# Optimization experiments

Hardware: AMD Instinct MI355X
Metric: run time of the kernel (lower is better)

The kernel has to match this reference:

```python
import jax, jax.numpy as jnp
import numpy as np

B, C, HH, WW = 256, 1024, 7, 7
S = HH * WW            # 49 tokens
D = 1024               # hidden_size
L = 2                  # encoder_layers (nhead arg, swapped in source)
H = 2                  # attention heads (num_layers arg, swapped in source)
HD = D // H            # 512 head dim
FF = 1024              # encoder_ffn_dim
OUT = 1024             # head output
EPS = 1e-5


def setup_inputs() -> dict:
    key = jax.random.key(0)
    ks = jax.random.split(key, 10)
    n = lambda k, shape: jax.random.normal(k, shape, jnp.float32) * 0.02
    return dict(
        x=jax.random.normal(ks[0], (B, C, HH, WW), jnp.float32),
        pos_emb=n(ks[1], (S, D)),
        ln1_s=jnp.ones((L, D), jnp.float32), ln1_b=jnp.zeros((L, D), jnp.float32),
        wq=n(ks[2], (L, D, D)), wk=n(ks[3], (L, D, D)),
        wv=n(ks[4], (L, D, D)), wo=n(ks[5], (L, D, D)),
        ln2_s=jnp.ones((L, D), jnp.float32), ln2_b=jnp.zeros((L, D), jnp.float32),
        w1=n(ks[6], (L, D, FF)), b1=jnp.zeros((L, FF), jnp.float32),
        w2=n(ks[7], (L, FF, D)), b2=jnp.zeros((L, D), jnp.float32),
        lnf_s=jnp.ones((D,), jnp.float32), lnf_b=jnp.zeros((D,), jnp.float32),
        head_w=n(ks[8], (S * D, OUT)), head_b=jnp.zeros((OUT,), jnp.float32),
    )


def _ln(x, s, b):
    m = jnp.mean(x, axis=-1, keepdims=True)
    v = jnp.var(x, axis=-1, keepdims=True)
    return (x - m) * jax.lax.rsqrt(v + EPS) * s + b


def reference(x, pos_emb, ln1_s, ln1_b, wq, wk, wv, wo, ln2_s, ln2_b,
              w1, b1, w2, b2, lnf_s, lnf_b, head_w, head_b):
    b = x.shape[0]
    # flatten HxW then permute -> [B, S, D] token sequence
    h = x.reshape(b, C, S).transpose(0, 2, 1)
    # BigBirdPegasus encoder: learned pos emb added to inputs_embeds (no scaling path)
    h = h + pos_emb[None, :, :]
    scale = 1.0 / jnp.sqrt(jnp.float32(HD))
    for i in range(L):
        # --- self-attention block (pre-LN); seq_len=49 triggers original_full attention ---
        r = h
        hn = _ln(h, ln1_s[i], ln1_b[i])
        q = (hn @ wq[i]).reshape(b, S, H, HD)
        k = (hn @ wk[i]).reshape(b, S, H, HD)
        v = (hn @ wv[i]).reshape(b, S, H, HD)
        scores = jnp.einsum('bqhd,bkhd->bhqk', q, k) * scale
        attn = jax.nn.softmax(scores, axis=-1)
        ctx = jnp.einsum('bhqk,bkhd->bqhd', attn, v).reshape(b, S, D)
        h = r + ctx @ wo[i]
        # --- feed-forward block (pre-LN, gelu_new) ---
        r = h
        hn = _ln(h, ln2_s[i], ln2_b[i])
        hn = jax.nn.gelu(hn @ w1[i] + b1[i], approximate=True)
        h = r + hn @ w2[i] + b2[i]
    # BigBirdPegasus applies layernorm_embedding AFTER the layer stack
    h = _ln(h, lnf_s, lnf_b)
    # flatten + linear + relu head
    out = jax.nn.relu(h.reshape(b, S * D) @ head_w + head_b)
    return out
```

## Files before the change

kernel.cpp:

```cpp
#include <hip/hip_runtime.h>
#include <hip/hip_bf16.h>
#include <stdint.h>

#define Bq 256
#define Sq 49
#define Dq 1024
#define Hq 2
#define HDq 512
#define Mq (Bq*Sq)
#define KHEADq (Sq*Dq)
#define STq 3072

typedef unsigned short u16;
typedef short bf16x8 __attribute__((ext_vector_type(8)));
typedef float f32x4 __attribute__((ext_vector_type(4)));

__device__ inline u16 f2bf(float f){
  union { float f; uint32_t u; } c; c.f = f;
  uint32_t r = c.u + 0x7FFFu + ((c.u >> 16) & 1u);
  return (u16)(r >> 16);
}
__device__ inline float bf2f(u16 h){
  union { uint32_t u; float f; } c; c.u = ((uint32_t)h) << 16;
  return c.f;
}

#define GLOAD_LDS16(gp, lp) \
  __builtin_amdgcn_global_load_lds((__attribute__((address_space(1))) void*)(gp), \
                                   (__attribute__((address_space(3))) void*)(lp), 16, 0, 0)
#define MFMA16(a,b,c) __builtin_amdgcn_mfma_f32_16x16x32_bf16(a,b,c,0,0,0)

__global__ __launch_bounds__(256) void prep_kernel(const float* __restrict__ x,
    const float* __restrict__ pos, u16* __restrict__ h){
  __shared__ float t[49*129];
  int b = blockIdx.x, c0 = blockIdx.y*128;
  int tid = threadIdx.x, lane = tid & 63, wave = tid >> 6;
  const float* xb = x + (size_t)b*(Dq*Sq) + (size_t)c0*Sq;
  #pragma unroll
  for(int i=0;i<32;i++){
    int cc = wave + i*4;
    if(lane < Sq) t[lane*129 + cc] = xb[(size_t)cc*Sq + lane];
  }
  __syncthreads();
  #pragma unroll
  for(int p=0;p<25;p++){
    int idx = p*256 + tid;
    int s = idx >> 7, cc = idx & 127;
    if(s < Sq)
      h[((size_t)b*Sq + s)*Dq + c0 + cc] = f2bf(t[s*129 + cc] + pos[s*Dq + c0 + cc]);
  }
}

__global__ __launch_bounds__(256) void ln_kernel(const u16* __restrict__ hin,
    const float* __restrict__ sc, const float* __restrict__ bi, u16* __restrict__ outp){
  int wave = threadIdx.x >> 6, lane = threadIdx.x & 63;
  int row = blockIdx.x*4 + wave;
  const u16* p = hin + (size_t)row*Dq + lane*16;
  uint4 t0 = *(const uint4*)p;
  uint4 t1 = *(const uint4*)(p + 8);
  float v[16];
  {
    uint32_t wds[8] = {t0.x,t0.y,t0.z,t0.w,t1.x,t1.y,t1.z,t1.w};
    #pragma unroll
    for(int i=0;i<8;i++){
      v[2*i]   = bf2f((u16)(wds[i] & 0xffff));
      v[2*i+1] = bf2f((u16)(wds[i] >> 16));
    }
  }
  float s=0.f, sq=0.f;
  #pragma unroll
  for(int i=0;i<16;i++){ s += v[i]; sq += v[i]*v[i]; }
  #pragma unroll
  for(int o=32;o>=1;o>>=1){ s += __shfl_xor(s,o); sq += __shfl_xor(sq,o); }
  float mean = s * (1.f/Dq);
  float var  = sq * (1.f/Dq) - mean*mean;
  float rs = rsqrtf(var + 1e-5f);
  int c0 = lane*16;
  uint32_t w[8];
  #pragma unroll
  for(int i=0;i<8;i++){
    u16 lo = f2bf((v[2*i]   - mean)*rs*sc[c0+2*i]   + bi[c0+2*i]);
    u16 hi = f2bf((v[2*i+1] - mean)*rs*sc[c0+2*i+1] + bi[c0+2*i+1]);
    w[i] = (uint32_t)lo | ((uint32_t)hi << 16);
  }
  uint4* ob = (uint4*)(outp + (size_t)row*Dq + c0);
  ob[0] = make_uint4(w[0],w[1],w[2],w[3]);
  ob[1] = make_uint4(w[4],w[5],w[6],w[7]);
}

__global__ void transp_all(const float* __restrict__ wq, const float* __restrict__ wk,
    const float* __restrict__ wv, const float* __restrict__ wo,
    const float* __restrict__ w1, const float* __restrict__ w2, u16* __restrict__ outp){
  __shared__ float t[32][33];
  int slot = blockIdx.z; int l = slot / 6, j = slot - l*6;
  const float* srcs[6] = {wq,wk,wv,wo,w1,w2};
  const float* in = srcs[j] + (size_t)l*Dq*Dq;
  u16* o = outp + (size_t)slot*Dq*Dq;
  int k0 = blockIdx.x*32, n0 = blockIdx.y*32;
  int tx = threadIdx.x, ty = threadIdx.y;
  #pragma unroll
  for(int i=0;i<4;i++) t[ty+8*i][tx] = in[(size_t)(k0+ty+8*i)*Dq + n0+tx];
  __syncthreads();
  #pragma unroll
  for(int i=0;i<4;i++) o[(size_t)(n0+ty+8*i)*Dq + k0+tx] = f2bf(t[tx][ty+8*i]);
}

template<int EPI>
__global__ __launch_bounds__(512, 2) void gemm_nt2(
    const u16* __restrict__ A, int lda,
    const u16* __restrict__ Bt, int ldb,
    void* __restrict__ Cout, const u16* __restrict__ resid,
    const float* __restrict__ bias, int ldc)
{
  __shared__ u16 lds[65536];
  int tid = threadIdx.x, lane = tid & 63;
  int wave = tid >> 6;
  int wm = wave >> 2, wn = wave & 3;
  int l15 = lane & 15, l4 = lane >> 4;
  int swz = (l15 & 7) << 4;

  int gx = gridDim.x, nwg = gx*gridDim.y;
  int orig = blockIdx.y*gx + blockIdx.x;
  int qq = nwg >> 3, rr = nwg & 7;
  int xcd = orig & 7, idx = orig >> 3;
  int wgid = (xcd < rr ? xcd*(qq+1) : rr*(qq+1) + (xcd-rr)*qq) + idx;
  int bx = wgid % gx, by = wgid / gx;
  int m0 = by*256, n0 = bx*256;

  int srow = tid >> 3, scolb = (tid & 7) * 16;
  int scolx = scolb ^ ((srow & 7) << 4);
  auto stage2 = [&](int d, int kt, int h){
    #pragma unroll
    for(int cc=0; cc<2; cc++){
      int c = 2*h + cc;
      if(c < 4){
        int row = c*64 + srow;
        const u16* src = A + (size_t)(m0+row)*lda + kt*64 + (scolx>>1);
        GLOAD_LDS16(src, &lds[d*16384 + c*4096 + tid*8]);
      } else {
        int c4 = c - 4;
        int row = c4*64 + srow;
        const u16* src = Bt + (size_t)(n0+row)*ldb + kt*64 + (scolx>>1);
        GLOAD_LDS16(src, &lds[32768 + d*16384 + c4*4096 + tid*8]);
      }
    }
  };
  auto rdA = [&](int d, int i, int s)->bf16x8{
    int row = wm*128 + i*16 + l15;
    int byt = row*128 + ((s*64 + l4*16) ^ swz);
    return *(const bf16x8*)((const char*)lds + d*32768 + byt);
  };
  auto rdB = [&](int d, int n, int s)->bf16x8{
    int row = wn*64 + n*16 + l15;
    int byt = row*128 + ((s*64 + l4*16) ^ swz);
    return *(const bf16x8*)((const char*)lds + 65536 + d*32768 + byt);
  };

  f32x4 acc[8][4] = {};

  #pragma unroll
  for(int h=0;h<4;h++) stage2(0, 0, h);

  for(int t=0; t<16; ++t){
    int d = t & 1;
    bf16x8 bfr[4][2];
    if(t < 15){
      stage2(d^1, t+1, 0);
      asm volatile("s_waitcnt vmcnt(2)" ::: "memory");
    } else {
      asm volatile("s_waitcnt vmcnt(0)" ::: "memory");
    }
    __builtin_amdgcn_sched_barrier(0);
    __builtin_amdgcn_s_barrier();
    bfr[0][0]=rdB(d,0,0); bfr[0][1]=rdB(d,0,1);
    bfr[1][0]=rdB(d,1,0); bfr[1][1]=rdB(d,1,1);
    bf16x8 a0s0=rdA(d,0,0), a0s1=rdA(d,0,1), a1s0=rdA(d,1,0), a1s1=rdA(d,1,1);
    __builtin_amdgcn_s_setprio(1);
    acc[0][0]=MFMA16(a0s0,bfr[0][0],acc[0][0]); acc[0][0]=MFMA16(a0s1,bfr[0][1],acc[0][0]);
    acc[0][1]=MFMA16(a0s0,bfr[1][0],acc[0][1]); acc[0][1]=MFMA16(a0s1,bfr[1][1],acc[0][1]);
    acc[1][0]=MFMA16(a1s0,bfr[0][0],acc[1][0]); acc[1][0]=MFMA16(a1s1,bfr[0][1],acc[1][0]);
    acc[1][1]=MFMA16(a1s0,bfr[1][0],acc[1][1]); acc[1][1]=MFMA16(a1s1,bfr[1][1],acc[1][1]);
    __builtin_amdgcn_s_setprio(0);
    __builtin_amdgcn_s_barrier();
    bfr[2][0]=rdB(d,2,0); bfr[2][1]=rdB(d,2,1);
    bfr[3][0]=rdB(d,3,0); bfr[3][1]=rdB(d,3,1);
    if(t < 15) stage2(d^1, t+1, 1);
    __builtin_amdgcn_s_barrier();
    __builtin_amdgcn_s_setprio(1);
    acc[0][2]=MFMA16(a0s0,bfr[2][0],acc[0][2]); acc[0][2]=MFMA16(a0s1,bfr[2][1],acc[0][2]);
    acc[0][3]=MFMA16(a0s0,bfr[3][0],acc[0][3]); acc[0][3]=MFMA16(a0s1,bfr[3][1],acc[0][3]);
    acc[1][2]=MFMA16(a1s0,bfr[2][0],acc[1][2]); acc[1][2]=MFMA16(a1s1,bfr[2][1],acc[1][2]);
    acc[1][3]=MFMA16(a1s0,bfr[3][0],acc[1][3]); acc[1][3]=MFMA16(a1s1,bfr[3][1],acc[1][3]);
    __builtin_amdgcn_s_setprio(0);
    __builtin_amdgcn_s_barrier();
    #pragma unroll
    for(int q=1;q<4;q++){
      bf16x8 c0s0=rdA(d,2*q,0), c0s1=rdA(d,2*q,1), c1s0=rdA(d,2*q+1,0), c1s1=rdA(d,2*q+1,1);
      if(t < 15 && q < 3) stage2(d^1, t+1, q+1);
      __builtin_amdgcn_s_barrier();
      __builtin_amdgcn_s_setprio(1);
      #pragma unroll
      for(int n=0;n<4;n++){
        acc[2*q][n]   = MFMA16(c0s0, bfr[n][0], acc[2*q][n]);
        acc[2*q][n]   = MFMA16(c0s1, bfr[n][1], acc[2*q][n]);
        acc[2*q+1][n] = MFMA16(c1s0, bfr[n][0], acc[2*q+1][n]);
        acc[2*q+1][n] = MFMA16(c1s1, bfr[n][1], acc[2*q+1][n]);
      }
      __builtin_amdgcn_s_setprio(0);
      __builtin_amdgcn_s_barrier();
    }
  }

  if constexpr (EPI == 1){
    float* slotf = (float*)((char*)lds + wave*4096);
    float bv[4];
    #pragma unroll
    for(int n=0;n<4;n++) bv[n] = bias ? bias[n0 + wn*64 + n*16 + l15] : 0.f;
    #pragma unroll
    for(int i=0;i<8;i++){
      #pragma unroll
      for(int n=0;n<4;n++)
        #pragma unroll
        for(int r=0;r<4;r++)
          slotf[(l4*4+r)*64 + n*16 + l15] = acc[i][n][r] + bv[n];
      #pragma unroll
      for(int st=0;st<2;st++){
        int u = st*64 + lane;
        int row = u >> 3, c8 = (u & 7)*8;
        f32x4 lo = *(const f32x4*)&slotf[row*64 + c8];
        f32x4 hi = *(const f32x4*)&slotf[row*64 + c8 + 4];
        size_t o = (size_t)(m0 + wm*128 + i*16 + row)*ldc + n0 + wn*64 + c8;
        bf16x8 rb = *(const bf16x8*)(resid + o);
        bf16x8 ov;
        #pragma unroll
        for(int j=0;j<4;j++){
          ov[j]   = (short)f2bf(lo[j] + bf2f((u16)rb[j]));
          ov[4+j] = (short)f2bf(hi[j] + bf2f((u16)rb[4+j]));
        }
        *(bf16x8*)((u16*)Cout + o) = ov;
      }
    }
  } else {
    u16* slot = (u16*)((char*)lds + wave*2048);
    float bv[4];
    if constexpr (EPI == 2){
      #pragma unroll
      for(int n=0;n<4;n++) bv[n] = bias[n0 + wn*64 + n*16 + l15];
    }
    #pragma unroll
    for(int i=0;i<8;i++){
      #pragma unroll
      for(int n=0;n<4;n++)
        #pragma unroll
        for(int r=0;r<4;r++){
          float va = acc[i][n][r];
          u16 ov;
          if constexpr (EPI == 0){
            ov = f2bf(va);
          } else {
            float xg = va + bv[n];
            float tg = tanhf(0.79788456080286536f*(xg + 0.044715f*xg*xg*xg));
            ov = f2bf(0.5f*xg*(1.f+tg));
          }
          slot[(l4*4+r)*64 + n*16 + l15] = ov;
        }
      #pragma unroll
      for(int st=0;st<2;st++){
        int u = st*64 + lane;
        int row = u >> 3, c8 = (u & 7)*8;
        bf16x8 v8 = *(const bf16x8*)&slot[row*64 + c8];
        *(bf16x8*)((u16*)Cout + (size_t)(m0 + wm*128 + i*16 + row)*ldc + n0 + wn*64 + c8) = v8;
      }
    }
  }
}

__global__ __launch_bounds__(256) void gemm_head(
    const u16* __restrict__ A, const float* __restrict__ W,
    float* __restrict__ parts)
{
  __shared__ u16 sA[128*32];
  __shared__ float sC[4][1024];
  int tid = threadIdx.x, lane = tid & 63;
  int wave = tid >> 6;
  int wm = wave >> 1, wn = wave & 1;
  int l15 = lane & 15, l4 = lane >> 4;
  int nwg = gridDim.x*gridDim.y*gridDim.z;
  int orig = (blockIdx.z*gridDim.y + blockIdx.y)*gridDim.x + blockIdx.x;
  int cpx = nwg >> 3;
  int swz = (orig & 7)*cpx + (orig >> 3);
  int bx = swz & 7, by = (swz >> 3) & 1, z = swz >> 4;
  int m0 = by*128, n0 = bx*128;
  size_t abase = (size_t)m0*KHEADq + (size_t)z*1024;
  f32x4 acc[4][4] = {};
  const float* wp = W + ((size_t)z*1024 + (size_t)l4*8)*1024 + n0 + wn*64 + l15;
  for(int kt=0;kt<32;kt++){
    #pragma unroll
    for(int c=0;c<2;c++){
      int s2 = c*256+tid;
      GLOAD_LDS16(A + abase + (size_t)(s2>>2)*KHEADq + kt*32 + (s2&3)*8, &sA[s2*8]);
    }
    float wreg[4][8];
    #pragma unroll
    for(int f=0;f<4;f++)
      #pragma unroll
      for(int jj=0;jj<8;jj++)
        wreg[f][jj] = wp[(size_t)(kt*32+jj)*1024 + f*16];
    bf16x8 bfr[4];
    #pragma unroll
    for(int f=0;f<4;f++){
      bf16x8 bv;
      #pragma unroll
      for(int jj=0;jj<8;jj++)
        bv[jj] = __builtin_bit_cast(short, __float2bfloat16(wreg[f][jj]));
      bfr[f] = bv;
    }
    __syncthreads();
    bf16x8 af[4];
    #pragma unroll
    for(int f=0;f<4;f++)
      af[f] = *(const bf16x8*)&sA[(wm*64 + f*16 + l15)*32 + l4*8];
    #pragma unroll
    for(int i=0;i<4;i++)
      #pragma unroll
      for(int j=0;j<4;j++)
        acc[i][j] = MFMA16(af[i], bfr[j], acc[i][j]);
    __syncthreads();
  }
  float* base = parts + (size_t)z*(Bq*1024);
  #pragma unroll
  for(int i=0;i<4;i++){
    #pragma unroll
    for(int j=0;j<4;j++)
      #pragma unroll
      for(int r=0;r<4;r++)
        sC[wave][(l4*4+r)*64 + j*16 + l15] = acc[i][j][r];
    #pragma unroll
    for(int st=0;st<4;st++){
      int u = st*64 + lane;
      int row = u >> 4, c4 = (u & 15)*4;
      f32x4 v4 = *(const f32x4*)&sC[wave][row*64 + c4];
      *(f32x4*)(base + (size_t)(m0+wm*64+i*16+row)*1024 + n0+wn*64+c4) = v4;
    }
  }
}

__global__ __launch_bounds__(256) void attn_kernel(u16* __restrict__ qkv)
{
  __shared__ float sS[64][65];
  __shared__ u16 sP[64][64];
  int bh = blockIdx.x;
  int b = bh >> 1, h = bh & 1;
  int tid = threadIdx.x, lane = tid & 63, wave = tid >> 6;
  int l15 = lane & 15, l4 = lane >> 4;
  f32x4 zero4 = {0.f,0.f,0.f,0.f};
  bf16x8 zb = {0,0,0,0,0,0,0,0};
  f32x4 acc[4];
  #pragma unroll
  for(int i=0;i<4;i++) acc[i] = zero4;
  int srow = wave*16 + l15;
  const u16* qp = qkv + (size_t)(b*Sq + srow)*STq + h*HDq + l4*8;
  const u16* kbase = qkv + (size_t)b*Sq*STq + Dq + h*HDq + l4*8;
  for(int kt=0;kt<16;kt++){
    bf16x8 aq = (srow < Sq) ? *(const bf16x8*)(qp + kt*32) : zb;
    #pragma unroll
    for(int fn=0;fn<4;fn++){
      int s2 = fn*16 + l15;
      bf16x8 bk = (s2 < Sq) ? *(const bf16x8*)(kbase + (size_t)s2*STq + kt*32) : zb;
      acc[fn] = MFMA16(aq, bk, acc[fn]);
    }
  }
  const float scale = 0.04419417382415922f;
  #pragma unroll
  for(int fn=0;fn<4;fn++)
    #pragma unroll
    for(int r=0;r<4;r++)
      sS[wave*16 + l4*4 + r][fn*16 + l15] = acc[fn][r]*scale;
  __syncthreads();
  if(tid < 64){
    float mx = -1e30f;
    for(int j=0;j<Sq;j++) mx = fmaxf(mx, sS[tid][j]);
    float sum = 0.f;
    for(int j=0;j<Sq;j++){ float e = __expf(sS[tid][j]-mx); sS[tid][j]=e; sum+=e; }
    float inv = 1.f/sum;
    for(int j=0;j<64;j++) sP[tid][j] = (j<Sq)? f2bf(sS[tid][j]*inv) : (u16)0;
  }
  __syncthreads();
  bf16x8 ap[2];
  #pragma unroll
  for(int kt2=0;kt2<2;kt2++)
    ap[kt2] = *(const bf16x8*)&sP[wave*16 + l15][kt2*32 + l4*8];
  const u16* vbp = qkv + (size_t)b*Sq*STq + 2*Dq + h*HDq + l15;
  u16* cb = qkv + (size_t)b*Sq*STq + h*HDq;
  for(int fn=0;fn<32;fn++){
    f32x4 c4 = zero4;
    #pragma unroll
    for(int kt2=0;kt2<2;kt2++){
      const u16* vp = vbp + fn*16 + (size_t)(kt2*32 + l4*8)*STq;
      bf16x8 bv;
      #pragma unroll
      for(int jj=0;jj<8;jj++) bv[jj] = (short)vp[(size_t)jj*STq];
      c4 = MFMA16(ap[kt2], bv, c4);
    }
    #pragma unroll
    for(int r=0;r<4;r++){
      int s = wave*16 + l4*4 + r;
      if(s < Sq) cb[(size_t)s*STq + fn*16 + l15] = f2bf(c4[r]);
    }
  }
}

__global__ __launch_bounds__(256) void head_finalize(const float* __restrict__ parts,
    const float* __restrict__ hb, float* __restrict__ outp){
  int idx = blockIdx.x*256 + threadIdx.x;
  float s = hb[idx & 1023];
  #pragma unroll
  for(int z=0;z<49;z++) s += parts[(size_t)z*(Bq*1024) + idx];
  outp[idx] = fmaxf(s, 0.f);
}

extern "C" void kernel_launch(void* const* d_in, const int* in_sizes, int n_in,
                              void* d_out, int out_size, void* d_ws, size_t ws_size,
                              hipStream_t stream) {
  (void)in_sizes; (void)n_in; (void)out_size;
  const float* x    = (const float*)d_in[0];
  const float* pos  = (const float*)d_in[1];
  const float* ln1s = (const float*)d_in[2];
  const float* ln1b = (const float*)d_in[3];
  const float* wq   = (const float*)d_in[4];
  const float* wk   = (const float*)d_in[5];
  const float* wv   = (const float*)d_in[6];
  const float* wo   = (const float*)d_in[7];
  const float* ln2s = (const float*)d_in[8];
  const float* ln2b = (const float*)d_in[9];
  const float* w1   = (const float*)d_in[10];
  const float* b1   = (const float*)d_in[11];
  const float* w2   = (const float*)d_in[12];
  const float* b2   = (const float*)d_in[13];
  const float* lnfs = (const float*)d_in[14];
  const float* lnfb = (const float*)d_in[15];
  const float* hw   = (const float*)d_in[16];
  const float* hb   = (const float*)d_in[17];
  float* out = (float*)d_out;

  char* ws = (char*)d_ws;
  size_t off = 0;
  auto carve = [&](size_t n) -> char* { char* p = ws + off; off += (n + 255) & ~(size_t)255; return p; };
  u16*  h     = (u16*) carve((size_t)Mq*Dq*2);
  u16*  act0  = (u16*) carve((size_t)Mq*Dq*2);
  u16*  act1  = (u16*) carve((size_t)Mq*Dq*2);
  u16*  qkv   = (u16*) carve((size_t)(Mq+16)*STq*2);
  u16*  wT    = (u16*) carve((size_t)12*Dq*Dq*2);
  float* parts= (float*)qkv;
  if (off > ws_size) return;

  hipMemsetAsync(qkv + (size_t)Mq*STq, 0, (size_t)16*STq*2, stream);

  prep_kernel<<<dim3(Bq, 8), 256, 0, stream>>>(x, pos, h);
  transp_all<<<dim3(32,32,12), dim3(32,8), 0, stream>>>(wq, wk, wv, wo, w1, w2, wT);

  dim3 gg(4, Mq/256);
  dim3 gq(12, Mq/256);
  for(int l=0;l<2;l++){
    u16* qkvT = wT + (size_t)(l*6+0)*Dq*Dq;
    u16* woT  = wT + (size_t)(l*6+3)*Dq*Dq;
    u16* w1T  = wT + (size_t)(l*6+4)*Dq*Dq;
    u16* w2T  = wT + (size_t)(l*6+5)*Dq*Dq;

    ln_kernel<<<Mq/4, 256, 0, stream>>>(h, ln1s + l*Dq, ln1b + l*Dq, act0);
    gemm_nt2<0><<<gq, 512, 0, stream>>>(act0, Dq, qkvT, Dq, qkv, nullptr, nullptr, STq);
    attn_kernel<<<Bq*Hq, 256, 0, stream>>>(qkv);
    gemm_nt2<1><<<gg, 512, 0, stream>>>(qkv, STq, woT, Dq, h, h, nullptr, Dq);
    ln_kernel<<<Mq/4, 256, 0, stream>>>(h, ln2s + l*Dq, ln2b + l*Dq, act0);
    gemm_nt2<2><<<gg, 512, 0, stream>>>(act0, Dq, w1T, Dq, act1, nullptr, b1 + l*Dq, Dq);
    gemm_nt2<1><<<gg, 512, 0, stream>>>(act1, Dq, w2T, Dq, h, h, b2 + l*Dq, Dq);
  }

  ln_kernel<<<Mq/4, 256, 0, stream>>>(h, lnfs, lnfb, act0);
  gemm_head<<<dim3(8,2,49), 256, 0, stream>>>(act0, hw, parts);
  head_finalize<<<1024, 256, 0, stream>>>(parts, hb, out);
}
```

Baseline: 683.6 us.

## Fold pre-LayerNorm into GEMMs via row stats and weight-side scale/bias terms

```diff
diff --git a/kernel.cpp b/kernel.cpp
--- a/kernel.cpp
+++ b/kernel.cpp
@@ -31,7 +31,7 @@
 #define MFMA16(a,b,c) __builtin_amdgcn_mfma_f32_16x16x32_bf16(a,b,c,0,0,0)
 
 __global__ __launch_bounds__(256) void prep_kernel(const float* __restrict__ x,
-    const float* __restrict__ pos, u16* __restrict__ h){
+    const float* __restrict__ pos, u16* __restrict__ h, float2* __restrict__ pstat){
   __shared__ float t[49*129];
   int b = blockIdx.x, c0 = blockIdx.y*128;
   int tid = threadIdx.x, lane = tid & 63, wave = tid >> 6;
@@ -46,8 +46,20 @@
   for(int p=0;p<25;p++){
     int idx = p*256 + tid;
     int s = idx >> 7, cc = idx & 127;
-    if(s < Sq)
-      h[((size_t)b*Sq + s)*Dq + c0 + cc] = f2bf(t[s*129 + cc] + pos[s*Dq + c0 + cc]);
+    if(s < Sq){
+      float hv = t[s*129 + cc] + pos[s*Dq + c0 + cc];
+      h[((size_t)b*Sq + s)*Dq + c0 + cc] = f2bf(hv);
+      t[s*129 + cc] = hv;
+    }
+  }
+  __syncthreads();
+  int r = tid >> 2, qd = tid & 3;
+  if(r < Sq){
+    float S=0.f, Q=0.f;
+    for(int cc=qd; cc<128; cc+=4){ float vv = t[r*129+cc]; S+=vv; Q+=vv*vv; }
+    S += __shfl_xor(S,1); Q += __shfl_xor(Q,1);
+    S += __shfl_xor(S,2); Q += __shfl_xor(Q,2);
+    if(qd==0){ float2 pp; pp.x=S; pp.y=Q; pstat[(size_t)blockIdx.y*Mq + b*Sq + r] = pp; }
   }
 }
 
@@ -90,19 +102,43 @@
 
 __global__ void transp_all(const float* __restrict__ wq, const float* __restrict__ wk,
     const float* __restrict__ wv, const float* __restrict__ wo,
-    const float* __restrict__ w1, const float* __restrict__ w2, u16* __restrict__ outp){
+    const float* __restrict__ w1, const float* __restrict__ w2,
+    const float* __restrict__ ln1s, const float* __restrict__ ln2s, u16* __restrict__ outp){
   __shared__ float t[32][33];
   int slot = blockIdx.z; int l = slot / 6, j = slot - l*6;
   const float* srcs[6] = {wq,wk,wv,wo,w1,w2};
   const float* in = srcs[j] + (size_t)l*Dq*Dq;
+  const float* sc = (j<3) ? (ln1s + l*Dq) : (j==4 ? (ln2s + l*Dq) : nullptr);
   u16* o = outp + (size_t)slot*Dq*Dq;
   int k0 = blockIdx.x*32, n0 = blockIdx.y*32;
   int tx = threadIdx.x, ty = threadIdx.y;
   #pragma unroll
   for(int i=0;i<4;i++) t[ty+8*i][tx] = in[(size_t)(k0+ty+8*i)*Dq + n0+tx];
   __syncthreads();
-  #pragma unroll
-  for(int i=0;i<4;i++) o[(size_t)(n0+ty+8*i)*Dq + k0+tx] = f2bf(t[tx][ty+8*i]);
+  float sck = sc ? sc[k0+tx] : 1.f;
+  #pragma unroll
+  for(int i=0;i<4;i++) o[(size_t)(n0+ty+8*i)*Dq + k0+tx] = f2bf(t[tx][ty+8*i] * sck);
+}
+
+__global__ __launch_bounds__(256) void uv_kernel(const float* __restrict__ wq,
+    const float* __restrict__ wk, const float* __restrict__ wv, const float* __restrict__ w1,
+    const float* __restrict__ ln1s, const float* __restrict__ ln1b,
+    const float* __restrict__ ln2s, const float* __restrict__ ln2b, float* __restrict__ uvbuf){
+  int bid = blockIdx.x;
+  int l = bid >> 4, chunk = bid & 15;
+  int col = chunk*256 + threadIdx.x;
+  int j = col >> 10, n = col & 1023;
+  const float* srcs[4] = {wq, wk, wv, w1};
+  const float* src = srcs[j] + (size_t)l*Dq*Dq;
+  const float* sc = (j<3 ? ln1s : ln2s) + l*Dq;
+  const float* bi = (j<3 ? ln1b : ln2b) + l*Dq;
+  float u=0.f, v=0.f;
+  for(int k=0;k<Dq;k++){
+    float val = src[(size_t)k*Dq + n];
+    u += sc[k]*val; v += bi[k]*val;
+  }
+  uvbuf[((size_t)l*4096 + col)*2]   = u;
+  uvbuf[((size_t)l*4096 + col)*2+1] = v;
 }
 
 template<int EPI>
@@ -110,7 +146,9 @@
     const u16* __restrict__ A, int lda,
     const u16* __restrict__ Bt, int ldb,
     void* __restrict__ Cout, const u16* __restrict__ resid,
-    const float* __restrict__ bias, int ldc)
+    const float* __restrict__ bias, int ldc,
+    const float2* __restrict__ pstat_in, int nchunk,
+    const float* __restrict__ uvp, float2* __restrict__ pstat_out)
 {
   __shared__ u16 lds[65536];
   int tid = threadIdx.x, lane = tid & 63;
@@ -212,6 +250,7 @@
   }
 
   if constexpr (EPI == 1){
+    float2* statsS = (float2*)((char*)lds + 49152);
     float* slotf = (float*)((char*)lds + wave*4096);
     float bv[4];
     #pragma unroll
@@ -231,21 +270,52 @@
         f32x4 hi = *(const f32x4*)&slotf[row*64 + c8 + 4];
         size_t o = (size_t)(m0 + wm*128 + i*16 + row)*ldc + n0 + wn*64 + c8;
         bf16x8 rb = *(const bf16x8*)(resid + o);
-        bf16x8 ov;
+        bf16x8 ov; float fs=0.f, fq=0.f;
         #pragma unroll
         for(int j=0;j<4;j++){
-          ov[j]   = (short)f2bf(lo[j] + bf2f((u16)rb[j]));
-          ov[4+j] = (short)f2bf(hi[j] + bf2f((u16)rb[4+j]));
+          float a_ = lo[j] + bf2f((u16)rb[j]);
+          float b_ = hi[j] + bf2f((u16)rb[4+j]);
+          ov[j]   = (short)f2bf(a_);
+          ov[4+j] = (short)f2bf(b_);
+          fs += a_ + b_; fq += a_*a_ + b_*b_;
         }
         *(bf16x8*)((u16*)Cout + o) = ov;
+        fs += __shfl_xor(fs,1); fq += __shfl_xor(fq,1);
+        fs += __shfl_xor(fs,2); fq += __shfl_xor(fq,2);
+        fs += __shfl_xor(fs,4); fq += __shfl_xor(fq,4);
+        if((lane&7)==0){
+          float2 pp; pp.x=fs; pp.y=fq;
+          statsS[(wm*128 + i*16 + st*8 + (lane>>3))*4 + wn] = pp;
+        }
       }
     }
+    __syncthreads();
+    if(tid < 256){
+      float S=0.f, Q=0.f;
+      #pragma unroll
+      for(int w2_=0;w2_<4;w2_++){ float2 pp = statsS[tid*4+w2_]; S+=pp.x; Q+=pp.y; }
+      float2 pp; pp.x=S; pp.y=Q;
+      pstat_out[(size_t)bx*Mq + m0 + tid] = pp;
+    }
   } else {
+    float2* lstat = (float2*)((char*)lds + 49152);
+    if(tid < 256){
+      float S=0.f, Q=0.f;
+      for(int c=0;c<nchunk;c++){ float2 pp = pstat_in[(size_t)c*Mq + m0 + tid]; S+=pp.x; Q+=pp.y; }
+      float mean = S*(1.f/1024.f);
+      float var  = Q*(1.f/1024.f) - mean*mean;
+      float2 sm; sm.x = rsqrtf(var + 1e-5f); sm.y = mean;
+      lstat[tid] = sm;
+    }
+    __syncthreads();
     u16* slot = (u16*)((char*)lds + wave*2048);
-    float bv[4];
-    if constexpr (EPI == 2){
-      #pragma unroll
-      for(int n=0;n<4;n++) bv[n] = bias[n0 + wn*64 + n*16 + l15];
+    float uvv[4][2], bv[4];
+    #pragma unroll
+    for(int n=0;n<4;n++){
+      int ncol = n0 + wn*64 + n*16 + l15;
+      float2 uv2 = ((const float2*)uvp)[ncol];
+      uvv[n][0] = uv2.x; uvv[n][1] = uv2.y;
+      if constexpr (EPI == 2) bv[n] = bias[ncol];
     }
     #pragma unroll
     for(int i=0;i<8;i++){
@@ -253,7 +323,8 @@
       for(int n=0;n<4;n++)
         #pragma unroll
         for(int r=0;r<4;r++){
-          float va = acc[i][n][r];
+          float2 sm = lstat[wm*128 + i*16 + l4*4 + r];
+          float va = sm.x*acc[i][n][r] - sm.x*sm.y*uvv[n][0] + uvv[n][1];
           u16 ov;
           if constexpr (EPI == 0){
             ov = f2bf(va);
@@ -377,13 +448,18 @@
     for(int r=0;r<4;r++)
       sS[wave*16 + l4*4 + r][fn*16 + l15] = acc[fn][r]*scale;
   __syncthreads();
-  if(tid < 64){
+  {
+    int r = tid >> 2, qd = tid & 3;
     float mx = -1e30f;
-    for(int j=0;j<Sq;j++) mx = fmaxf(mx, sS[tid][j]);
+    for(int j=qd;j<Sq;j+=4) mx = fmaxf(mx, sS[r][j]);
+    mx = fmaxf(mx, __shfl_xor(mx,1));
+    mx = fmaxf(mx, __shfl_xor(mx,2));
     float sum = 0.f;
-    for(int j=0;j<Sq;j++){ float e = __expf(sS[tid][j]-mx); sS[tid][j]=e; sum+=e; }
+    for(int j=qd;j<Sq;j+=4){ float e = __expf(sS[r][j]-mx); sS[r][j]=e; sum+=e; }
+    sum += __shfl_xor(sum,1);
+    sum += __shfl_xor(sum,2);
     float inv = 1.f/sum;
-    for(int j=0;j<64;j++) sP[tid][j] = (j<Sq)? f2bf(sS[tid][j]*inv) : (u16)0;
+    for(int j=qd;j<64;j+=4) sP[r][j] = (j<Sq)? f2bf(sS[r][j]*inv) : (u16)0;
   }
   __syncthreads();
   bf16x8 ap[2];
@@ -446,18 +522,21 @@
   char* ws = (char*)d_ws;
   size_t off = 0;
   auto carve = [&](size_t n) -> char* { char* p = ws + off; off += (n + 255) & ~(size_t)255; return p; };
-  u16*  h     = (u16*) carve((size_t)Mq*Dq*2);
-  u16*  act0  = (u16*) carve((size_t)Mq*Dq*2);
-  u16*  act1  = (u16*) carve((size_t)Mq*Dq*2);
-  u16*  qkv   = (u16*) carve((size_t)(Mq+16)*STq*2);
-  u16*  wT    = (u16*) carve((size_t)12*Dq*Dq*2);
-  float* parts= (float*)qkv;
+  u16*   h     = (u16*)  carve((size_t)Mq*Dq*2);
+  u16*   act0  = (u16*)  carve((size_t)Mq*Dq*2);
+  u16*   act1  = (u16*)  carve((size_t)Mq*Dq*2);
+  u16*   qkv   = (u16*)  carve((size_t)(Mq+16)*STq*2);
+  u16*   wT    = (u16*)  carve((size_t)12*Dq*Dq*2);
+  float2* pstat= (float2*)carve((size_t)8*Mq*sizeof(float2));
+  float* uvbuf = (float*)carve((size_t)2*4096*2*4);
+  float* parts = (float*)qkv;
   if (off > ws_size) return;
 
   hipMemsetAsync(qkv + (size_t)Mq*STq, 0, (size_t)16*STq*2, stream);
 
-  prep_kernel<<<dim3(Bq, 8), 256, 0, stream>>>(x, pos, h);
-  transp_all<<<dim3(32,32,12), dim3(32,8), 0, stream>>>(wq, wk, wv, wo, w1, w2, wT);
+  prep_kernel<<<dim3(Bq, 8), 256, 0, stream>>>(x, pos, h, pstat);
+  transp_all<<<dim3(32,32,12), dim3(32,8), 0, stream>>>(wq, wk, wv, wo, w1, w2, ln1s, ln2s, wT);
+  uv_kernel<<<32, 256, 0, stream>>>(wq, wk, wv, w1, ln1s, ln1b, ln2s, ln2b, uvbuf);
 
   dim3 gg(4, Mq/256);
   dim3 gq(12, Mq/256);
@@ -466,14 +545,18 @@
     u16* woT  = wT + (size_t)(l*6+3)*Dq*Dq;
     u16* w1T  = wT + (size_t)(l*6+4)*Dq*Dq;
     u16* w2T  = wT + (size_t)(l*6+5)*Dq*Dq;
-
-    ln_kernel<<<Mq/4, 256, 0, stream>>>(h, ln1s + l*Dq, ln1b + l*Dq, act0);
-    gemm_nt2<0><<<gq, 512, 0, stream>>>(act0, Dq, qkvT, Dq, qkv, nullptr, nullptr, STq);
+    const float* uvq = uvbuf + (size_t)l*8192;
+    const float* uv1 = uvbuf + (size_t)l*8192 + 3072*2;
+
+    gemm_nt2<0><<<gq, 512, 0, stream>>>(h, Dq, qkvT, Dq, qkv, nullptr, nullptr, STq,
+                                        pstat, (l==0)?8:4, uvq, nullptr);
     attn_kernel<<<Bq*Hq, 256, 0, stream>>>(qkv);
-    gemm_nt2<1><<<gg, 512, 0, stream>>>(qkv, STq, woT, Dq, h, h, nullptr, Dq);
-    ln_kernel<<<Mq/4, 256, 0, stream>>>(h, ln2s + l*Dq, ln2b + l*Dq, act0);
-    gemm_nt2<2><<<gg, 512, 0, stream>>>(act0, Dq, w1T, Dq, act1, nullptr, b1 + l*Dq, Dq);
-    gemm_nt2<1><<<gg, 512, 0, stream>>>(act1, Dq, w2T, Dq, h, h, b2 + l*Dq, Dq);
+    gemm_nt2<1><<<gg, 512, 0, stream>>>(qkv, STq, woT, Dq, h, h, nullptr, Dq,
+                                        nullptr, 0, nullptr, pstat);
+    gemm_nt2<2><<<gg, 512, 0, stream>>>(h, Dq, w1T, Dq, act1, nullptr, b1 + l*Dq, Dq,
+                                        pstat, 4, uv1, nullptr);
+    gemm_nt2<1><<<gg, 512, 0, stream>>>(act1, Dq, w2T, Dq, h, h, b2 + l*Dq, Dq,
+                                        nullptr, 0, nullptr, pstat);
   }
 
   ln_kernel<<<Mq/4, 256, 0, stream>>>(h, lnfs, lnfb, act0);
```

Result: slower. 742.1 us (+8.6%).
